# Kernel tuning notes

Hardware: AMD Instinct MI355X
Metric: run time of the kernel (lower is better)

## Reference

```python
import jax, jax.numpy as jnp
import numpy as np

N_NODES = 50000
N_EDGES = 800000
NODE_DIM = 256
EDGE_DIM = 64
NUM_REL = 4
HID = 512      # hidden_dims[0]
LAST = 128     # last_dim_size
BATCH = 16384
EPS = 1e-10    # torchdrug RelationalGraphConv degree-normalization eps


def _glorot(k, shape):
    fan_in = shape[-1]
    return jax.random.normal(k, shape, jnp.float32) / np.sqrt(fan_in).astype(np.float32)


def setup_inputs() -> dict:
    key = jax.random.key(0)
    ks = jax.random.split(key, 20)
    inp = {}
    inp["inputs"] = jax.random.randint(ks[0], (BATCH, 3), 0, N_NODES, dtype=jnp.int32)
    inp["node_feature"] = jax.random.normal(ks[1], (N_NODES, NODE_DIM), jnp.float32)
    inp["edge_feature"] = jax.random.normal(ks[2], (N_EDGES, EDGE_DIM), jnp.float32)
    inp["edge_src"] = jax.random.randint(ks[3], (N_EDGES,), 0, N_NODES, dtype=jnp.int32)
    inp["edge_dst"] = jax.random.randint(ks[4], (N_EDGES,), 0, N_NODES, dtype=jnp.int32)
    inp["edge_rel"] = jax.random.randint(ks[5], (N_EDGES,), 0, NUM_REL, dtype=jnp.int32)
    # RGCN layer 1: 256 -> 512
    inp["We1"] = _glorot(ks[6], (NODE_DIM, EDGE_DIM)); inp["be1"] = jnp.zeros((NODE_DIM,), jnp.float32)
    inp["Wl1"] = _glorot(ks[7], (HID, NUM_REL * NODE_DIM)); inp["bl1"] = jnp.zeros((HID,), jnp.float32)
    inp["Ws1"] = _glorot(ks[8], (HID, NODE_DIM)); inp["bs1"] = jnp.zeros((HID,), jnp.float32)
    # RGCN layer 2: 512 -> 128
    inp["We2"] = _glorot(ks[9], (HID, EDGE_DIM)); inp["be2"] = jnp.zeros((HID,), jnp.float32)
    inp["Wl2"] = _glorot(ks[10], (LAST, NUM_REL * HID)); inp["bl2"] = jnp.zeros((LAST,), jnp.float32)
    inp["Ws2"] = _glorot(ks[11], (LAST, HID)); inp["bs2"] = jnp.zeros((LAST,), jnp.float32)
    # ccle_mlp: edge_dim -> 256 -> 128
    inp["Wc1"] = _glorot(ks[12], (256, EDGE_DIM)); inp["bc1"] = jnp.zeros((256,), jnp.float32)
    inp["Wc2"] = _glorot(ks[13], (LAST, 256)); inp["bc2"] = jnp.zeros((LAST,), jnp.float32)
    # final MLP: 3*128 -> 128 -> 64 -> 1
    inp["Wf1"] = _glorot(ks[14], (128, 3 * LAST)); inp["bf1"] = jnp.zeros((128,), jnp.float32)
    inp["Wf2"] = _glorot(ks[15], (64, 128)); inp["bf2"] = jnp.zeros((64,), jnp.float32)
    inp["Wf3"] = _glorot(ks[16], (1, 64)); inp["bf3"] = jnp.zeros((1,), jnp.float32)
    return inp


def _rgcn_layer(x, edge_src, edge_dst, edge_rel, edge_feat, We, be, Wl, bl, Ws, bs):
    """torchdrug RelationalGraphConv: message = x[src] + edge_linear(edge_feat);
    per-(node,relation) mean aggregation; combine = linear(update) + self_loop(x); relu."""
    in_dim = x.shape[1]
    msg = x[edge_src] + edge_feat @ We.T + be                      # [E, in_dim]
    seg = edge_dst * NUM_REL + edge_rel                            # [E]
    agg = jax.ops.segment_sum(msg, seg, num_segments=N_NODES * NUM_REL)
    cnt = jax.ops.segment_sum(jnp.ones((msg.shape[0], 1), msg.dtype), seg,
                              num_segments=N_NODES * NUM_REL)
    upd = (agg / (cnt + EPS)).reshape(N_NODES, NUM_REL * in_dim)   # [N, R*in_dim]
    return jax.nn.relu(upd @ Wl.T + bl + x @ Ws.T + bs)


def reference(inputs, node_feature, edge_feature, edge_src, edge_dst, edge_rel,
              We1, be1, Wl1, bl1, Ws1, bs1,
              We2, be2, Wl2, bl2, Ws2, bs2,
              Wc1, bc1, Wc2, bc2,
              Wf1, bf1, Wf2, bf2, Wf3, bf3):
    d1, d2, ctx = inputs[:, 0], inputs[:, 1], inputs[:, 2]
    h = _rgcn_layer(node_feature, edge_src, edge_dst, edge_rel, edge_feature,
                    We1, be1, Wl1, bl1, Ws1, bs1)
    h = _rgcn_layer(h, edge_src, edge_dst, edge_rel, edge_feature,
                    We2, be2, Wl2, bl2, Ws2, bs2)
    x1 = h[d1]                                                     # [B, 128]
    x2 = h[d2]                                                     # [B, 128]
    ef = edge_feature[ctx]                                         # [B, 64]
    x3 = jax.nn.relu(ef @ Wc1.T + bc1) @ Wc2.T + bc2               # [B, 128]
    x = jnp.concatenate([x1, x2, x3], axis=1)                      # [B, 384]
    x = jax.nn.relu(x @ Wf1.T + bf1)
    x = jax.nn.relu(x @ Wf2.T + bf2)
    return x @ Wf3.T + bf3                                         # [B, 1]
```

## Files before the change

kernel.cpp:

```cpp
#include <hip/hip_runtime.h>
#include <hip/hip_bf16.h>

#define N_NODES 50000
#define N_EDGES 800000
#define NODE_DIM 256
#define EDGE_DIM 64
#define NUM_REL 4
#define HID 512
#define LAST 128
#define BATCH 16384
#define EPS 1e-10f
#define NSEG (N_NODES * NUM_REL)

#define K1 1600
#define K2 832

typedef __bf16 bf16_t;
typedef __attribute__((ext_vector_type(8))) __bf16 bf16x8;
typedef __attribute__((ext_vector_type(4))) __bf16 bf16x4;
typedef __attribute__((ext_vector_type(2))) __bf16 bf16x2;
typedef __attribute__((ext_vector_type(4))) float f32x4;

typedef __attribute__((address_space(1))) const unsigned int g_u32;
typedef __attribute__((address_space(3))) unsigned int l_u32;
static __device__ __forceinline__ void gload16(const void* g, void* l) {
    __builtin_amdgcn_global_load_lds((g_u32*)g, (l_u32*)l, 16, 0, 0);
}

__global__ __launch_bounds__(256) void hist_kernel(
    const int* __restrict__ edst, const int* __restrict__ erel, int* __restrict__ hist)
{
    int e = blockIdx.x * 256 + threadIdx.x;
    if (e >= N_EDGES) return;
    atomicAdd(&hist[edst[e] * NUM_REL + erel[e]], 1);
}

#define SCAN_B 2048
__global__ __launch_bounds__(256) void scan1(
    const int* __restrict__ in, int* __restrict__ out, int* __restrict__ bsum, int n)
{
    __shared__ int sh[256];
    int base = blockIdx.x * SCAN_B + threadIdx.x * 8;
    int v[8]; int s = 0;
#pragma unroll
    for (int i = 0; i < 8; ++i) {
        int idx = base + i;
        v[i] = s;
        s += (idx < n) ? in[idx] : 0;
    }
    sh[threadIdx.x] = s;
    __syncthreads();
    for (int off = 1; off < 256; off <<= 1) {
        int t = (threadIdx.x >= off) ? sh[threadIdx.x - off] : 0;
        __syncthreads();
        sh[threadIdx.x] += t;
        __syncthreads();
    }
    int texcl = (threadIdx.x == 0) ? 0 : sh[threadIdx.x - 1];
#pragma unroll
    for (int i = 0; i < 8; ++i) {
        int idx = base + i;
        if (idx < n) out[idx] = texcl + v[i];
    }
    if (threadIdx.x == 255) bsum[blockIdx.x] = sh[255];
}

__global__ void scan2(int* bsum, int nb)
{
    if (threadIdx.x == 0 && blockIdx.x == 0) {
        int s = 0;
        for (int i = 0; i < nb; ++i) { int t = bsum[i]; bsum[i] = s; s += t; }
    }
}

__global__ __launch_bounds__(256) void scan3(int* __restrict__ out, int* __restrict__ cursor,
                                             const int* __restrict__ bsum, int n)
{
    int idx = blockIdx.x * SCAN_B + threadIdx.x * 8;
    int add = bsum[blockIdx.x];
#pragma unroll
    for (int i = 0; i < 8; ++i)
        if (idx + i < n) {
            int v = out[idx + i] + add;
            out[idx + i] = v;
            cursor[idx + i] = v;
        }
}

__global__ __launch_bounds__(256) void csr_fill(
    const int* __restrict__ edst, const int* __restrict__ erel, const int* __restrict__ esrc,
    int* __restrict__ cursor,
    int* __restrict__ csr_src, int* __restrict__ csr_eid)
{
    int e = blockIdx.x * 256 + threadIdx.x;
    if (e >= N_EDGES) return;
    int seg = edst[e] * NUM_REL + erel[e];
    int pos = atomicAdd(&cursor[seg], 1);
    csr_src[pos] = esrc[e];
    csr_eid[pos] = e;
}

__global__ __launch_bounds__(256) void prep_small(
    const float* __restrict__ Wc1, const float* __restrict__ Wc2,
    const float* __restrict__ Wf1, const float* __restrict__ Wf2,
    const float* __restrict__ bl1, const float* __restrict__ bs1,
    const float* __restrict__ bl2, const float* __restrict__ bs2,
    bf16_t* __restrict__ Wc1b, bf16_t* __restrict__ Wc2b,
    bf16_t* __restrict__ Wf1b, bf16_t* __restrict__ Wf2b,
    float* __restrict__ bias12, float* __restrict__ bias22)
{
    int i = blockIdx.x * 256 + threadIdx.x;
    const float* src; bf16_t* dst; int base;
    if (i < 4096)        { src = Wc1; dst = Wc1b; base = 0; }
    else if (i < 12288)  { src = Wc2; dst = Wc2b; base = 4096; }
    else if (i < 24576)  { src = Wf1; dst = Wf1b; base = 12288; }
    else if (i < 26624)  { src = Wf2; dst = Wf2b; base = 24576; }
    else {
        int j = i - 26624;
        if (j < 512) bias12[j] = bl1[j] + bs1[j];
        else if (j < 640) bias22[j - 512] = bl2[j - 512] + bs2[j - 512];
        return;
    }
    int k = i - base;
    float4 v = ((const float4*)src)[k];
    bf16x4 o;
    o[0] = (bf16_t)v.x; o[1] = (bf16_t)v.y; o[2] = (bf16_t)v.z; o[3] = (bf16_t)v.w;
    ((bf16x4*)dst)[k] = o;
}

__global__ __launch_bounds__(256) void xconv_k(const float* __restrict__ x, bf16_t* __restrict__ A1,
                                               bf16_t* __restrict__ xb)
{
    int i = blockIdx.x * 256 + threadIdx.x;
    int n = i >> 6;
    int c4 = i & 63;
    float4 v = ((const float4*)(x + (size_t)n * 256))[c4];
    bf16x4 o;
    o[0] = (bf16_t)v.x; o[1] = (bf16_t)v.y; o[2] = (bf16_t)v.z; o[3] = (bf16_t)v.w;
    *(bf16x4*)(A1 + (size_t)n * K1 + 1280 + c4 * 4) = o;
    *(bf16x4*)(xb + (size_t)n * 256 + c4 * 4) = o;
}

__global__ __launch_bounds__(256) void prep_w1cat(
    const float* __restrict__ Wl1, const float* __restrict__ We1,
    const float* __restrict__ Ws1, const float* __restrict__ be1, bf16_t* __restrict__ W1cat)
{
    int j = blockIdx.x;
    int t = threadIdx.x;
    const float* wrow = Wl1 + (size_t)j * 1024;
    bf16_t* out = W1cat + (size_t)j * K1;
    for (int c = t; c < 1024; c += 256) out[c] = (bf16_t)wrow[c];
    {
        int r = t >> 6, e = t & 63;
        float s = 0.f;
        const float* wr = wrow + r * 256;
        for (int c = 0; c < 256; ++c) s += wr[c] * We1[c * 64 + e];
        out[1024 + t] = (bf16_t)s;
    }
    if (t < 256) out[1280 + t] = (bf16_t)Ws1[(size_t)j * 256 + t];
    if (t < 4) {
        float s = 0.f;
        const float* wr = wrow + t * 256;
        for (int c = 0; c < 256; ++c) s += wr[c] * be1[c];
        out[1536 + t] = (bf16_t)s;
    }
    if (t >= 4 && t < 64) out[1536 + t] = (bf16_t)0.f;
}

__global__ __launch_bounds__(256) void prep_w2cat(
    const float* __restrict__ Wl2, const float* __restrict__ We2,
    const float* __restrict__ Ws2, const float* __restrict__ be2, bf16_t* __restrict__ W2cat)
{
    int j = blockIdx.x;
    int t = threadIdx.x;
    const float* wrow = Wl2 + (size_t)j * 2048;
    bf16_t* out = W2cat + (size_t)j * K2;
    {
        int r = t >> 6, e = t & 63;
        float s = 0.f;
        const float* wr = wrow + r * 512;
        for (int k = 0; k < 512; ++k) s += wr[k] * We2[k * 64 + e];
        out[t] = (bf16_t)s;
    }
    for (int c = t; c < 512; c += 256) out[256 + c] = (bf16_t)Ws2[(size_t)j * 512 + c];
    if (t < 4) {
        float s = 0.f;
        const float* wr = wrow + t * 512;
        for (int k = 0; k < 512; ++k) s += wr[k] * be2[k];
        out[768 + t] = (bf16_t)s;
    }
    if (t >= 4 && t < 64) out[768 + t] = (bf16_t)0.f;
}

__global__ __launch_bounds__(256) void prep_w2p(const float* __restrict__ Wl2, bf16_t* __restrict__ W2p)
{
    int idx = blockIdx.x * 256 + threadIdx.x;
    int row = idx >> 9, k = idx & 511;
    int j = row & 127, r = row >> 7;
    W2p[idx] = (bf16_t)Wl2[(size_t)j * 2048 + r * 512 + k];
}

__global__ __launch_bounds__(256) void agg1(
    const float* __restrict__ ef, const bf16_t* __restrict__ xb,
    const int* __restrict__ csr_src, const int* __restrict__ csr_eid,
    const int* __restrict__ offs, const int* __restrict__ hist,
    bf16_t* __restrict__ A1, bf16_t* __restrict__ A2)
{
    int n = blockIdx.x;
    int w = threadIdx.x >> 6;
    int lane = threadIdx.x & 63;
    int half = lane >> 5;
    int l32 = lane & 31;
    int seg = n * NUM_REL + w;
    int beg = offs[seg], ct = hist[seg];

    float xs[8] = {0.f, 0.f, 0.f, 0.f, 0.f, 0.f, 0.f, 0.f};
    float es0 = 0.f, es1 = 0.f;

    int i = 0;
    for (; i + 4 <= ct; i += 4) {
        int sA = csr_src[beg + i + half];
        int sB = csr_src[beg + i + 2 + half];
        int eA = csr_eid[beg + i + half];
        int eB = csr_eid[beg + i + 2 + half];
        bf16x8 vA = *(const bf16x8*)(xb + (size_t)sA * 256 + l32 * 8);
        bf16x8 vB = *(const bf16x8*)(xb + (size_t)sB * 256 + l32 * 8);
        float2 fA = *(const float2*)(ef + (size_t)eA * 64 + l32 * 2);
        float2 fB = *(const float2*)(ef + (size_t)eB * 64 + l32 * 2);
#pragma unroll
        for (int j = 0; j < 8; ++j) xs[j] += (float)vA[j] + (float)vB[j];
        es0 += fA.x + fB.x;
        es1 += fA.y + fB.y;
    }
    for (; i + 2 <= ct; i += 2) {
        int sA = csr_src[beg + i + half];
        int eA = csr_eid[beg + i + half];
        bf16x8 vA = *(const bf16x8*)(xb + (size_t)sA * 256 + l32 * 8);
        float2 fA = *(const float2*)(ef + (size_t)eA * 64 + l32 * 2);
#pragma unroll
        for (int j = 0; j < 8; ++j) xs[j] += (float)vA[j];
        es0 += fA.x;
        es1 += fA.y;
    }
    if (i < ct && half == 0) {
        int sA = csr_src[beg + i];
        int eA = csr_eid[beg + i];
        bf16x8 vA = *(const bf16x8*)(xb + (size_t)sA * 256 + l32 * 8);
        float2 fA = *(const float2*)(ef + (size_t)eA * 64 + l32 * 2);
#pragma unroll
        for (int j = 0; j < 8; ++j) xs[j] += (float)vA[j];
        es0 += fA.x;
        es1 += fA.y;
    }
#pragma unroll
    for (int j = 0; j < 8; ++j) xs[j] += __shfl_xor(xs[j], 32);
    es0 += __shfl_xor(es0, 32);
    es1 += __shfl_xor(es1, 32);

    float inv = 1.0f / ((float)ct + EPS);
    if (half == 0) {
        bf16x8 m;
#pragma unroll
        for (int j = 0; j < 8; ++j) m[j] = (bf16_t)(xs[j] * inv);
        *(bf16x8*)(A1 + (size_t)n * K1 + w * 256 + l32 * 8) = m;
        bf16x2 e2;
        e2[0] = (bf16_t)(es0 * inv);
        e2[1] = (bf16_t)(es1 * inv);
        *(bf16x2*)(A1 + (size_t)n * K1 + 1024 + w * 64 + l32 * 2) = e2;
        *(bf16x2*)(A2 + (size_t)n * K2 + w * 64 + l32 * 2) = e2;
    }
    if (lane == 0) {
        bf16_t fv = (bf16_t)((float)ct * inv);
        A1[(size_t)n * K1 + 1536 + w] = fv;
        A2[(size_t)n * K2 + 768 + w] = fv;
    }
    if (w == 3 && lane >= 4) {
        A1[(size_t)n * K1 + 1536 + lane] = (bf16_t)0.f;
        A2[(size_t)n * K2 + 768 + lane] = (bf16_t)0.f;
    }
}

__global__ __launch_bounds__(256) void agg2(
    const bf16_t* __restrict__ P, const int* __restrict__ csr_src,
    const int* __restrict__ offs, const int* __restrict__ hist,
    float* __restrict__ h2base)
{
    __shared__ float red[4][128];
    int n = blockIdx.x;
    int w = threadIdx.x >> 6;
    int lane = threadIdx.x & 63;
    int half = lane >> 5;
    int l32 = lane & 31;
    int seg = n * NUM_REL + w;
    int beg = offs[seg], ct = hist[seg];

    float s0 = 0.f, s1 = 0.f, s2 = 0.f, s3 = 0.f;
    int i = 0;
    for (; i + 4 <= ct; i += 4) {
        int a = csr_src[beg + i + half];
        int b = csr_src[beg + i + 2 + half];
        bf16x4 va = *(const bf16x4*)(P + (size_t)a * HID + w * 128 + l32 * 4);
        bf16x4 vb = *(const bf16x4*)(P + (size_t)b * HID + w * 128 + l32 * 4);
        s0 += (float)va[0] + (float)vb[0];
        s1 += (float)va[1] + (float)vb[1];
        s2 += (float)va[2] + (float)vb[2];
        s3 += (float)va[3] + (float)vb[3];
    }
    for (; i + 2 <= ct; i += 2) {
        int a = csr_src[beg + i + half];
        bf16x4 va = *(const bf16x4*)(P + (size_t)a * HID + w * 128 + l32 * 4);
        s0 += (float)va[0]; s1 += (float)va[1]; s2 += (float)va[2]; s3 += (float)va[3];
    }
    if (i < ct && half == 0) {
        int a = csr_src[beg + i];
        bf16x4 va = *(const bf16x4*)(P + (size_t)a * HID + w * 128 + l32 * 4);
        s0 += (float)va[0]; s1 += (float)va[1]; s2 += (float)va[2]; s3 += (float)va[3];
    }
    s0 += __shfl_xor(s0, 32);
    s1 += __shfl_xor(s1, 32);
    s2 += __shfl_xor(s2, 32);
    s3 += __shfl_xor(s3, 32);

    float inv = 1.0f / ((float)ct + EPS);
    if (half == 0) {
        red[w][l32 * 4 + 0] = s0 * inv;
        red[w][l32 * 4 + 1] = s1 * inv;
        red[w][l32 * 4 + 2] = s2 * inv;
        red[w][l32 * 4 + 3] = s3 * inv;
    }
    __syncthreads();
    int t = threadIdx.x;
    if (t < 128)
        h2base[(size_t)n * 128 + t] = red[0][t] + red[1][t] + red[2][t] + red[3][t];
}

template<int RELU, int ACC, int OUTBF>
__global__ __launch_bounds__(256) void gemm_bf16(
    const bf16_t* __restrict__ A, int lda,
    const bf16_t* __restrict__ W, int ldw,
    const float* __restrict__ Cin, int ldcin,
    const float* __restrict__ bias,
    void* __restrict__ Cout, int ldc,
    int M, int N, int K, int ncol)
{
    __shared__ char smem[65536];
    const int tid = threadIdx.x;

    const int nwg = gridDim.x;
    const int q8 = nwg >> 3, r8 = nwg & 7;
    const int xcd = blockIdx.x & 7, li = blockIdx.x >> 3;
    const int wgid = (xcd < r8 ? xcd * (q8 + 1) : r8 * (q8 + 1) + (xcd - r8) * q8) + li;

    const int row0 = (wgid / ncol) * 128;
    const int col0 = (wgid % ncol) * 128;
    const int lane = tid & 63, wv = tid >> 6;

    const int rsub = lane >> 3;
    const int gchunk = (lane & 7) ^ rsub;
    const bf16_t* pa[4]; const bf16_t* pb[4];
    int lofs[4];
#pragma unroll
    for (int s = 0; s < 4; ++s) {
        int q = wv * 4 + s;
        int ar = row0 + q * 8 + rsub; if (ar >= M) ar = M - 1;
        int br = col0 + q * 8 + rsub; if (br >= N) br = N - 1;
        pa[s] = A + (size_t)ar * lda + gchunk * 8;
        pb[s] = W + (size_t)br * ldw + gchunk * 8;
        lofs[s] = q * 1024;
    }

    const int wm = wv >> 1, wn = wv & 1;
    const int r16 = lane & 15, kch = lane >> 4;
    const int sw = r16 & 7;

    f32x4 acc[4][4];
#pragma unroll
    for (int i = 0; i < 4; ++i)
#pragma unroll
        for (int j = 0; j < 4; ++j) acc[i][j] = (f32x4){0.f, 0.f, 0.f, 0.f};

#pragma unroll
    for (int s = 0; s < 4; ++s) {
        gload16(pa[s], smem + lofs[s]);
        gload16(pb[s], smem + 16384 + lofs[s]);
    }

    const int nk = K >> 6;
    int cur = 0;
    for (int it = 0; it < nk; ++it) {
        const int k0 = it << 6;
        if (it + 1 < nk) {
            char* nb = smem + ((cur ^ 1) << 15);
#pragma unroll
            for (int s = 0; s < 4; ++s) {
                gload16(pa[s] + k0 + 64, nb + lofs[s]);
                gload16(pb[s] + k0 + 64, nb + 16384 + lofs[s]);
            }
            asm volatile("s_waitcnt vmcnt(8)" ::: "memory");
        } else {
            asm volatile("s_waitcnt vmcnt(0)" ::: "memory");
        }
        __builtin_amdgcn_s_barrier();
        __builtin_amdgcn_sched_barrier(0);
        const char* As = smem + (cur << 15);
        const char* Bs = As + 16384;
#pragma unroll
        for (int t = 0; t < 2; ++t) {
            const int slot = ((t * 4 + kch) ^ sw) << 4;
            bf16x8 af[4], bfm[4];
#pragma unroll
            for (int i = 0; i < 4; ++i)
                af[i] = *(const bf16x8*)(As + (wm * 64 + i * 16 + r16) * 128 + slot);
#pragma unroll
            for (int j = 0; j < 4; ++j)
                bfm[j] = *(const bf16x8*)(Bs + (wn * 64 + j * 16 + r16) * 128 + slot);
#pragma unroll
            for (int i = 0; i < 4; ++i)
#pragma unroll
                for (int j = 0; j < 4; ++j)
                    acc[i][j] = __builtin_amdgcn_mfma_f32_16x16x32_bf16(af[i], bfm[j], acc[i][j], 0, 0, 0);
        }
        __builtin_amdgcn_s_barrier();
        cur ^= 1;
    }

    const int crow0 = row0 + wm * 64;
#pragma unroll
    for (int i = 0; i < 4; ++i) {
#pragma unroll
        for (int j = 0; j < 4; ++j) {
            int col = col0 + wn * 64 + j * 16 + r16;
            if (col >= N) continue;
            float bv = bias ? bias[col] : 0.f;
#pragma unroll
            for (int q = 0; q < 4; ++q) {
                int row = crow0 + i * 16 + kch * 4 + q;
                if (row >= M) continue;
                float v = acc[i][j][q] + bv;
                if (ACC) v += Cin[(size_t)row * ldcin + col];
                if (RELU) v = fmaxf(v, 0.f);
                if (OUTBF) ((bf16_t*)Cout)[(size_t)row * ldc + col] = (bf16_t)v;
                else       ((float*)Cout)[(size_t)row * ldc + col] = v;
            }
        }
    }
}

__global__ __launch_bounds__(256) void gemm_f1g(
    const int* __restrict__ inputs, const bf16_t* __restrict__ h2,
    const bf16_t* __restrict__ x3, const bf16_t* __restrict__ Wf1b,
    const float* __restrict__ bf1, bf16_t* __restrict__ f1)
{
    __shared__ char smem[65536];
    const int tid = threadIdx.x;
    const int nwg = gridDim.x;
    const int q8 = nwg >> 3;
    const int xcd = blockIdx.x & 7, li = blockIdx.x >> 3;
    const int wgid = xcd * q8 + li;
    const int row0 = wgid * 128;
    const int lane = tid & 63, wv = tid >> 6;

    const int rsub = lane >> 3;
    const int gchunk = (lane & 7) ^ rsub;
    const bf16_t* baseA[4][3];
    const bf16_t* pb[4];
    int lofs[4];
#pragma unroll
    for (int s = 0; s < 4; ++s) {
        int q = wv * 4 + s;
        int ar = row0 + q * 8 + rsub;
        int d1 = inputs[ar * 3 + 0];
        int d2 = inputs[ar * 3 + 1];
        baseA[s][0] = h2 + (size_t)d1 * 128 + gchunk * 8;
        baseA[s][1] = h2 + (size_t)d2 * 128 + gchunk * 8;
        baseA[s][2] = x3 + (size_t)ar * 128 + gchunk * 8;
        int br = q * 8 + rsub;
        pb[s] = Wf1b + (size_t)br * 384 + gchunk * 8;
        lofs[s] = q * 1024;
    }

    const int wm = wv >> 1, wn = wv & 1;
    const int r16 = lane & 15, kch = lane >> 4;
    const int sw = r16 & 7;

    f32x4 acc[4][4];
#pragma unroll
    for (int i = 0; i < 4; ++i)
#pragma unroll
        for (int j = 0; j < 4; ++j) acc[i][j] = (f32x4){0.f, 0.f, 0.f, 0.f};

#pragma unroll
    for (int s = 0; s < 4; ++s) {
        gload16(baseA[s][0], smem + lofs[s]);
        gload16(pb[s], smem + 16384 + lofs[s]);
    }

    int cur = 0;
#pragma unroll
    for (int it = 0; it < 6; ++it) {
        const int k0 = it << 6;
        if (it < 5) {
            const int kn = k0 + 64;
            const int reg = kn >> 7, off = kn & 127;
            char* nb = smem + ((cur ^ 1) << 15);
#pragma unroll
            for (int s = 0; s < 4; ++s) {
                gload16(baseA[s][reg] + off, nb + lofs[s]);
                gload16(pb[s] + kn, nb + 16384 + lofs[s]);
            }
            asm volatile("s_waitcnt vmcnt(8)" ::: "memory");
        } else {
            asm volatile("s_waitcnt vmcnt(0)" ::: "memory");
        }
        __builtin_amdgcn_s_barrier();
        __builtin_amdgcn_sched_barrier(0);
        const char* As = smem + (cur << 15);
        const char* Bs = As + 16384;
#pragma unroll
        for (int t = 0; t < 2; ++t) {
            const int slot = ((t * 4 + kch) ^ sw) << 4;
            bf16x8 af[4], bfm[4];
#pragma unroll
            for (int i = 0; i < 4; ++i)
                af[i] = *(const bf16x8*)(As + (wm * 64 + i * 16 + r16) * 128 + slot);
#pragma unroll
            for (int j = 0; j < 4; ++j)
                bfm[j] = *(const bf16x8*)(Bs + (wn * 64 + j * 16 + r16) * 128 + slot);
#pragma unroll
            for (int i = 0; i < 4; ++i)
#pragma unroll
                for (int j = 0; j < 4; ++j)
                    acc[i][j] = __builtin_amdgcn_mfma_f32_16x16x32_bf16(af[i], bfm[j], acc[i][j], 0, 0, 0);
        }
        __builtin_amdgcn_s_barrier();
        cur ^= 1;
    }

    const int crow0 = row0 + wm * 64;
#pragma unroll
    for (int i = 0; i < 4; ++i) {
#pragma unroll
        for (int j = 0; j < 4; ++j) {
            int col = wn * 64 + j * 16 + r16;
            if (col >= 128) continue;
            float bv = bf1[col];
#pragma unroll
            for (int q = 0; q < 4; ++q) {
                int row = crow0 + i * 16 + kch * 4 + q;
                float v = fmaxf(acc[i][j][q] + bv, 0.f);
                f1[(size_t)row * 128 + col] = (bf16_t)v;
            }
        }
    }
}

__global__ __launch_bounds__(256) void gather_ef(
    const int* __restrict__ inputs, const float* __restrict__ ef, bf16_t* __restrict__ ef_g)
{
    int i = blockIdx.x * 256 + threadIdx.x;
    int row = i >> 4, c4 = i & 15;
    int ctx = inputs[row * 3 + 2];
    float4 v = *(const float4*)(ef + (size_t)ctx * 64 + c4 * 4);
    bf16x4 o;
    o[0] = (bf16_t)v.x; o[1] = (bf16_t)v.y; o[2] = (bf16_t)v.z; o[3] = (bf16_t)v.w;
    *(bf16x4*)(ef_g + (size_t)row * 64 + c4 * 4) = o;
}

__global__ __launch_bounds__(256) void head_tail(
    const bf16_t* __restrict__ f1, const bf16_t* __restrict__ Wf2b,
    const float* __restrict__ bf2, const float* __restrict__ Wf3,
    const float* __restrict__ bf3, float* __restrict__ out)
{
    __shared__ bf16_t sf1[128 * 128];
    int blk = blockIdx.x;
    int tid = threadIdx.x;
    const bf16_t* gsrc = f1 + (size_t)blk * 128 * 128;
    for (int i = tid; i < 128 * 16; i += 256)
        ((bf16x8*)sf1)[i] = ((const bf16x8*)gsrc)[i];
    int lane = tid & 63, wv = tid >> 6;
    bf16x8 w[16];
#pragma unroll
    for (int c = 0; c < 16; ++c) w[c] = ((const bf16x8*)(Wf2b + lane * 128))[c];
    float bias2 = bf2[lane];
    float wf3 = Wf3[lane];
    float b3 = bf3[0];
    __syncthreads();
    for (int r = wv; r < 128; r += 4) {
        const bf16x8* frow = (const bf16x8*)(sf1 + r * 128);
        float acc = 0.f;
#pragma unroll
        for (int c = 0; c < 16; ++c) {
            bf16x8 fv = frow[c];
#pragma unroll
            for (int j = 0; j < 8; ++j) acc += (float)fv[j] * (float)w[c][j];
        }
        float v = fmaxf(acc + bias2, 0.f) * wf3;
#pragma unroll
        for (int off = 32; off > 0; off >>= 1) v += __shfl_down(v, off);
        if (lane == 0) out[blk * 128 + r] = v + b3;
    }
}

extern "C" void kernel_launch(void* const* d_in, const int* in_sizes, int n_in,
                              void* d_out, int out_size, void* d_ws, size_t ws_size,
                              hipStream_t stream)
{
    const int*   inputs       = (const int*)  d_in[0];
    const float* node_feature = (const float*)d_in[1];
    const float* edge_feature = (const float*)d_in[2];
    const int*   edge_src     = (const int*)  d_in[3];
    const int*   edge_dst     = (const int*)  d_in[4];
    const int*   edge_rel     = (const int*)  d_in[5];
    const float* We1 = (const float*)d_in[6];
    const float* be1 = (const float*)d_in[7];
    const float* Wl1 = (const float*)d_in[8];
    const float* bl1 = (const float*)d_in[9];
    const float* Ws1 = (const float*)d_in[10];
    const float* bs1 = (const float*)d_in[11];
    const float* We2 = (const float*)d_in[12];
    const float* be2 = (const float*)d_in[13];
    const float* Wl2 = (const float*)d_in[14];
    const float* bl2 = (const float*)d_in[15];
    const float* Ws2 = (const float*)d_in[16];
    const float* bs2 = (const float*)d_in[17];
    const float* Wc1 = (const float*)d_in[18];
    const float* bc1 = (const float*)d_in[19];
    const float* Wc2 = (const float*)d_in[20];
    const float* bc2 = (const float*)d_in[21];
    const float* Wf1 = (const float*)d_in[22];
    const float* bf1 = (const float*)d_in[23];
    const float* Wf2 = (const float*)d_in[24];
    const float* bf2 = (const float*)d_in[25];
    const float* Wf3 = (const float*)d_in[26];
    const float* bf3 = (const float*)d_in[27];
    float* out = (float*)d_out;

    char* p = (char*)d_ws;
    auto alloc = [&](size_t bytes) { char* r = p; p += (bytes + 255) & ~(size_t)255; return r; };
    int* hist     = (int*)alloc(NSEG * 4);
    int* offs     = (int*)alloc(NSEG * 4);
    int* cursor   = (int*)alloc(NSEG * 4);
    int* csr_src  = (int*)alloc(N_EDGES * 4);
    int* csr_eid  = (int*)alloc(N_EDGES * 4);
    int* bsums    = (int*)alloc(128 * 4);
    bf16_t* A1    = (bf16_t*)alloc((size_t)N_NODES * K1 * 2);
    bf16_t* A2    = (bf16_t*)alloc((size_t)N_NODES * K2 * 2);
    bf16_t* xb    = (bf16_t*)alloc((size_t)N_NODES * 256 * 2);
    bf16_t* Pbuf  = (bf16_t*)alloc((size_t)N_NODES * HID * 2);
    float*  h2base= (float*)alloc((size_t)N_NODES * 128 * 4);
    bf16_t* h2    = (bf16_t*)alloc((size_t)N_NODES * 128 * 2);
    bf16_t* W1cat = (bf16_t*)alloc((size_t)512 * K1 * 2);
    bf16_t* W2cat = (bf16_t*)alloc((size_t)128 * K2 * 2);
    bf16_t* W2p   = (bf16_t*)alloc((size_t)512 * 512 * 2);
    bf16_t* Wc1b  = (bf16_t*)alloc(256 * 64 * 2);
    bf16_t* Wc2b  = (bf16_t*)alloc(128 * 256 * 2);
    bf16_t* Wf1b  = (bf16_t*)alloc(128 * 384 * 2);
    bf16_t* Wf2b  = (bf16_t*)alloc(64 * 128 * 2);
    float*  bias12= (float*)alloc(512 * 4);
    float*  bias22= (float*)alloc(128 * 4);
    bf16_t* ef_g  = (bf16_t*)alloc((size_t)BATCH * 64 * 2);
    bf16_t* u3    = (bf16_t*)alloc((size_t)BATCH * 256 * 2);
    bf16_t* x3buf = (bf16_t*)alloc((size_t)BATCH * 128 * 2);
    bf16_t* f1    = (bf16_t*)alloc((size_t)BATCH * 128 * 2);

    hipMemsetAsync(hist, 0, NSEG * 4, stream);
    hist_kernel<<<(N_EDGES + 255) / 256, 256, 0, stream>>>(edge_dst, edge_rel, hist);
    int nscan = (NSEG + SCAN_B - 1) / SCAN_B;
    scan1<<<nscan, 256, 0, stream>>>(hist, offs, bsums, NSEG);
    scan2<<<1, 64, 0, stream>>>(bsums, nscan);
    scan3<<<nscan, 256, 0, stream>>>(offs, cursor, bsums, NSEG);
    csr_fill<<<(N_EDGES + 255) / 256, 256, 0, stream>>>(edge_dst, edge_rel, edge_src,
                                                        cursor, csr_src, csr_eid);

    prep_w1cat<<<512, 256, 0, stream>>>(Wl1, We1, Ws1, be1, W1cat);
    prep_w2cat<<<128, 256, 0, stream>>>(Wl2, We2, Ws2, be2, W2cat);
    prep_w2p<<<(512 * 512) / 256, 256, 0, stream>>>(Wl2, W2p);
    prep_small<<<(26624 + 640 + 255) / 256, 256, 0, stream>>>(
        Wc1, Wc2, Wf1, Wf2, bl1, bs1, bl2, bs2,
        Wc1b, Wc2b, Wf1b, Wf2b, bias12, bias22);
    xconv_k<<<(N_NODES * 64 + 255) / 256, 256, 0, stream>>>(node_feature, A1, xb);

    agg1<<<N_NODES, 256, 0, stream>>>(edge_feature, xb, csr_src, csr_eid, offs, hist, A1, A2);
    {
        int nrow = (N_NODES + 127) / 128, ncol = HID / 128;
        gemm_bf16<1, 0, 1><<<nrow * ncol, 256, 0, stream>>>(A1, K1, W1cat, K1, nullptr, 0, bias12,
                                                            A2 + 256, K2, N_NODES, HID, K1, ncol);
    }

    {
        int nrow = (N_NODES + 127) / 128, ncol = HID / 128;
        gemm_bf16<0, 0, 1><<<nrow * ncol, 256, 0, stream>>>(A2 + 256, K2, W2p, 512, nullptr, 0, nullptr,
                                                            Pbuf, HID, N_NODES, HID, 512, ncol);
    }
    agg2<<<N_NODES, 256, 0, stream>>>(Pbuf, csr_src, offs, hist, h2base);
    {
        int nrow = (N_NODES + 127) / 128;
        gemm_bf16<1, 1, 1><<<nrow, 256, 0, stream>>>(A2, K2, W2cat, K2, h2base, 128, bias22,
                                                     h2, 128, N_NODES, 128, K2, 1);
    }

    gather_ef<<<(BATCH * 16) / 256, 256, 0, stream>>>(inputs, edge_feature, ef_g);
    {
        gemm_bf16<1, 0, 1><<<(BATCH / 128) * 2, 256, 0, stream>>>(ef_g, 64, Wc1b, 64, nullptr, 0, bc1,
                                                                  u3, 256, BATCH, 256, 64, 2);
    }
    {
        gemm_bf16<0, 0, 1><<<BATCH / 128, 256, 0, stream>>>(u3, 256, Wc2b, 256, nullptr, 0, bc2,
                                                            x3buf, 128, BATCH, 128, 256, 1);
    }
    gemm_f1g<<<BATCH / 128, 256, 0, stream>>>(inputs, h2, x3buf, Wf1b, bf1, f1);
    head_tail<<<BATCH / 128, 256, 0, stream>>>(f1, Wf2b, bf2, Wf3, bf3, out);
}
```

Baseline: 694.0 us.

## Replace double-buffered 64-K GEMM pipeline with single-buffered 32-K tiles

Both bf16 GEMM kernels drop the double-buffered LDS pipeline with 64-wide K steps and use a single 16KB buffer with 32-wide K steps, synchronised by __syncthreads around each step. The LDS swizzle is reworked for 64-byte rows. This cuts LDS use per workgroup from 64KB to 16KB, which may let more workgroups share a CU. In exchange, global loads no longer overlap with MFMA work and each K step needs two barriers, so latency is exposed more often.

```diff
diff --git a/kernel.cpp b/kernel.cpp
--- a/kernel.cpp
+++ b/kernel.cpp
@@ -343,7 +343,7 @@
     void* __restrict__ Cout, int ldc,
     int M, int N, int K, int ncol)
 {
-    __shared__ char smem[65536];
+    __shared__ char smem[16384];
     const int tid = threadIdx.x;
 
     const int nwg = gridDim.x;
@@ -355,23 +355,31 @@
     const int col0 = (wgid % ncol) * 128;
     const int lane = tid & 63, wv = tid >> 6;
 
-    const int rsub = lane >> 3;
-    const int gchunk = (lane & 7) ^ rsub;
-    const bf16_t* pa[4]; const bf16_t* pb[4];
-    int lofs[4];
-#pragma unroll
-    for (int s = 0; s < 4; ++s) {
-        int q = wv * 4 + s;
-        int ar = row0 + q * 8 + rsub; if (ar >= M) ar = M - 1;
-        int br = col0 + q * 8 + rsub; if (br >= N) br = N - 1;
-        pa[s] = A + (size_t)ar * lda + gchunk * 8;
-        pb[s] = W + (size_t)br * ldw + gchunk * 8;
-        lofs[s] = q * 1024;
-    }
+    const int srow = lane >> 2;
+    const int gchunk = (lane & 3) ^ ((lane >> 3) & 3);
+    const bf16_t *pa0, *pa1, *pb0, *pb1;
+    {
+        int r0 = (wv * 2 + 0) * 16 + srow;
+        int r1 = (wv * 2 + 1) * 16 + srow;
+        int a0 = row0 + r0; if (a0 >= M) a0 = M - 1;
+        int a1 = row0 + r1; if (a1 >= M) a1 = M - 1;
+        int b0 = col0 + r0; if (b0 >= N) b0 = N - 1;
+        int b1 = col0 + r1; if (b1 >= N) b1 = N - 1;
+        pa0 = A + (size_t)a0 * lda + gchunk * 8;
+        pa1 = A + (size_t)a1 * lda + gchunk * 8;
+        pb0 = W + (size_t)b0 * ldw + gchunk * 8;
+        pb1 = W + (size_t)b1 * ldw + gchunk * 8;
+    }
+    char* As = smem;
+    char* Bs = smem + 8192;
+    char* lA0 = As + (wv * 2 + 0) * 1024;
+    char* lA1 = As + (wv * 2 + 1) * 1024;
+    char* lB0 = Bs + (wv * 2 + 0) * 1024;
+    char* lB1 = Bs + (wv * 2 + 1) * 1024;
 
     const int wm = wv >> 1, wn = wv & 1;
     const int r16 = lane & 15, kch = lane >> 4;
-    const int sw = r16 & 7;
+    const int slot = (kch ^ ((r16 >> 1) & 3)) << 4;
 
     f32x4 acc[4][4];
 #pragma unroll
@@ -379,49 +387,25 @@
 #pragma unroll
         for (int j = 0; j < 4; ++j) acc[i][j] = (f32x4){0.f, 0.f, 0.f, 0.f};
 
-#pragma unroll
-    for (int s = 0; s < 4; ++s) {
-        gload16(pa[s], smem + lofs[s]);
-        gload16(pb[s], smem + 16384 + lofs[s]);
-    }
-
-    const int nk = K >> 6;
-    int cur = 0;
-    for (int it = 0; it < nk; ++it) {
-        const int k0 = it << 6;
-        if (it + 1 < nk) {
-            char* nb = smem + ((cur ^ 1) << 15);
-#pragma unroll
-            for (int s = 0; s < 4; ++s) {
-                gload16(pa[s] + k0 + 64, nb + lofs[s]);
-                gload16(pb[s] + k0 + 64, nb + 16384 + lofs[s]);
-            }
-            asm volatile("s_waitcnt vmcnt(8)" ::: "memory");
-        } else {
-            asm volatile("s_waitcnt vmcnt(0)" ::: "memory");
-        }
-        __builtin_amdgcn_s_barrier();
-        __builtin_amdgcn_sched_barrier(0);
-        const char* As = smem + (cur << 15);
-        const char* Bs = As + 16384;
-#pragma unroll
-        for (int t = 0; t < 2; ++t) {
-            const int slot = ((t * 4 + kch) ^ sw) << 4;
-            bf16x8 af[4], bfm[4];
-#pragma unroll
-            for (int i = 0; i < 4; ++i)
-                af[i] = *(const bf16x8*)(As + (wm * 64 + i * 16 + r16) * 128 + slot);
+    for (int k0 = 0; k0 < K; k0 += 32) {
+        gload16(pa0 + k0, lA0);
+        gload16(pa1 + k0, lA1);
+        gload16(pb0 + k0, lB0);
+        gload16(pb1 + k0, lB1);
+        __syncthreads();
+        bf16x8 af[4], bfm[4];
+#pragma unroll
+        for (int i = 0; i < 4; ++i)
+            af[i] = *(const bf16x8*)(As + (wm * 64 + i * 16 + r16) * 64 + slot);
+#pragma unroll
+        for (int j = 0; j < 4; ++j)
+            bfm[j] = *(const bf16x8*)(Bs + (wn * 64 + j * 16 + r16) * 64 + slot);
+#pragma unroll
+        for (int i = 0; i < 4; ++i)
 #pragma unroll
             for (int j = 0; j < 4; ++j)
-                bfm[j] = *(const bf16x8*)(Bs + (wn * 64 + j * 16 + r16) * 128 + slot);
-#pragma unroll
-            for (int i = 0; i < 4; ++i)
-#pragma unroll
-                for (int j = 0; j < 4; ++j)
-                    acc[i][j] = __builtin_amdgcn_mfma_f32_16x16x32_bf16(af[i], bfm[j], acc[i][j], 0, 0, 0);
-        }
-        __builtin_amdgcn_s_barrier();
-        cur ^= 1;
+                acc[i][j] = __builtin_amdgcn_mfma_f32_16x16x32_bf16(af[i], bfm[j], acc[i][j], 0, 0, 0);
+        __syncthreads();
     }
 
     const int crow0 = row0 + wm * 64;
@@ -451,37 +435,46 @@
     const bf16_t* __restrict__ x3, const bf16_t* __restrict__ Wf1b,
     const float* __restrict__ bf1, bf16_t* __restrict__ f1)
 {
-    __shared__ char smem[65536];
+    __shared__ char smem[16384];
     const int tid = threadIdx.x;
     const int nwg = gridDim.x;
-    const int q8 = nwg >> 3;
+    const int q8n = nwg >> 3;
     const int xcd = blockIdx.x & 7, li = blockIdx.x >> 3;
-    const int wgid = xcd * q8 + li;
+    const int wgid = xcd * q8n + li;
     const int row0 = wgid * 128;
     const int lane = tid & 63, wv = tid >> 6;
 
-    const int rsub = lane >> 3;
-    const int gchunk = (lane & 7) ^ rsub;
-    const bf16_t* baseA[4][3];
-    const bf16_t* pb[4];
-    int lofs[4];
-#pragma unroll
-    for (int s = 0; s < 4; ++s) {
-        int q = wv * 4 + s;
-        int ar = row0 + q * 8 + rsub;
-        int d1 = inputs[ar * 3 + 0];
-        int d2 = inputs[ar * 3 + 1];
-        baseA[s][0] = h2 + (size_t)d1 * 128 + gchunk * 8;
-        baseA[s][1] = h2 + (size_t)d2 * 128 + gchunk * 8;
-        baseA[s][2] = x3 + (size_t)ar * 128 + gchunk * 8;
-        int br = q * 8 + rsub;
-        pb[s] = Wf1b + (size_t)br * 384 + gchunk * 8;
-        lofs[s] = q * 1024;
-    }
+    const int srow = lane >> 2;
+    const int gchunk = (lane & 3) ^ ((lane >> 3) & 3);
+    const bf16_t* baseA0[3];
+    const bf16_t* baseA1[3];
+    const bf16_t *pb0, *pb1;
+    {
+        int r0 = (wv * 2 + 0) * 16 + srow;
+        int r1 = (wv * 2 + 1) * 16 + srow;
+        int ar0 = row0 + r0;
+        int ar1 = row0 + r1;
+        int d10 = inputs[ar0 * 3 + 0], d20 = inputs[ar0 * 3 + 1];
+        int d11 = inputs[ar1 * 3 + 0], d21 = inputs[ar1 * 3 + 1];
+        baseA0[0] = h2 + (size_t)d10 * 128 + gchunk * 8;
+        baseA0[1] = h2 + (size_t)d20 * 128 + gchunk * 8;
+        baseA0[2] = x3 + (size_t)ar0 * 128 + gchunk * 8;
+        baseA1[0] = h2 + (size_t)d11 * 128 + gchunk * 8;
+        baseA1[1] = h2 + (size_t)d21 * 128 + gchunk * 8;
+        baseA1[2] = x3 + (size_t)ar1 * 128 + gchunk * 8;
+        pb0 = Wf1b + (size_t)r0 * 384 + gchunk * 8;
+        pb1 = Wf1b + (size_t)r1 * 384 + gchunk * 8;
+    }
+    char* As = smem;
+    char* Bs = smem + 8192;
+    char* lA0 = As + (wv * 2 + 0) * 1024;
+    char* lA1 = As + (wv * 2 + 1) * 1024;
+    char* lB0 = Bs + (wv * 2 + 0) * 1024;
+    char* lB1 = Bs + (wv * 2 + 1) * 1024;
 
     const int wm = wv >> 1, wn = wv & 1;
     const int r16 = lane & 15, kch = lane >> 4;
-    const int sw = r16 & 7;
+    const int slot = (kch ^ ((r16 >> 1) & 3)) << 4;
 
     f32x4 acc[4][4];
 #pragma unroll
@@ -490,50 +483,28 @@
         for (int j = 0; j < 4; ++j) acc[i][j] = (f32x4){0.f, 0.f, 0.f, 0.f};
 
 #pragma unroll
-    for (int s = 0; s < 4; ++s) {
-        gload16(baseA[s][0], smem + lofs[s]);
-        gload16(pb[s], smem + 16384 + lofs[s]);
-    }
-
-    int cur = 0;
-#pragma unroll
-    for (int it = 0; it < 6; ++it) {
-        const int k0 = it << 6;
-        if (it < 5) {
-            const int kn = k0 + 64;
-            const int reg = kn >> 7, off = kn & 127;
-            char* nb = smem + ((cur ^ 1) << 15);
-#pragma unroll
-            for (int s = 0; s < 4; ++s) {
-                gload16(baseA[s][reg] + off, nb + lofs[s]);
-                gload16(pb[s] + kn, nb + 16384 + lofs[s]);
-            }
-            asm volatile("s_waitcnt vmcnt(8)" ::: "memory");
-        } else {
-            asm volatile("s_waitcnt vmcnt(0)" ::: "memory");
-        }
-        __builtin_amdgcn_s_barrier();
-        __builtin_amdgcn_sched_barrier(0);
-        const char* As = smem + (cur << 15);
-        const char* Bs = As + 16384;
-#pragma unroll
-        for (int t = 0; t < 2; ++t) {
-            const int slot = ((t * 4 + kch) ^ sw) << 4;
-            bf16x8 af[4], bfm[4];
-#pragma unroll
-            for (int i = 0; i < 4; ++i)
-                af[i] = *(const bf16x8*)(As + (wm * 64 + i * 16 + r16) * 128 + slot);
+    for (int it = 0; it < 12; ++it) {
+        const int k0 = it * 32;
+        const int reg = k0 >> 7;
+        const int off = k0 & 127;
+        gload16(baseA0[reg] + off, lA0);
+        gload16(baseA1[reg] + off, lA1);
+        gload16(pb0 + k0, lB0);
+        gload16(pb1 + k0, lB1);
+        __syncthreads();
+        bf16x8 af[4], bfm[4];
+#pragma unroll
+        for (int i = 0; i < 4; ++i)
+            af[i] = *(const bf16x8*)(As + (wm * 64 + i * 16 + r16) * 64 + slot);
+#pragma unroll
+        for (int j = 0; j < 4; ++j)
+            bfm[j] = *(const bf16x8*)(Bs + (wn * 64 + j * 16 + r16) * 64 + slot);
+#pragma unroll
+        for (int i = 0; i < 4; ++i)
 #pragma unroll
             for (int j = 0; j < 4; ++j)
-                bfm[j] = *(const bf16x8*)(Bs + (wn * 64 + j * 16 + r16) * 128 + slot);
-#pragma unroll
-            for (int i = 0; i < 4; ++i)
-#pragma unroll
-                for (int j = 0; j < 4; ++j)
-                    acc[i][j] = __builtin_amdgcn_mfma_f32_16x16x32_bf16(af[i], bfm[j], acc[i][j], 0, 0, 0);
-        }
-        __builtin_amdgcn_s_barrier();
-        cur ^= 1;
+                acc[i][j] = __builtin_amdgcn_mfma_f32_16x16x32_bf16(af[i], bfm[j], acc[i][j], 0, 0, 0);
+        __syncthreads();
     }
 
     const int crow0 = row0 + wm * 64;
@@ -542,7 +513,6 @@
 #pragma unroll
         for (int j = 0; j < 4; ++j) {
             int col = wn * 64 + j * 16 + r16;
-            if (col >= 128) continue;
             float bv = bf1[col];
 #pragma unroll
             for (int q = 0; q < 4; ++q) {
```

Result: slower. 748.0 us (+7.8%).

## Add 256x256-tile triple-buffered GEMM kernel for the two large node GEMMs

Applied to the files above, without the earlier changes.

Introduces a new 512-thread GEMM kernel with 256x256 output tiles, a three-stage LDS ring buffer with BK=32, split A/B global loads interleaved with MFMA phases, and s_setprio around the MFMA blocks. It replaces the 128x128 kernel for the layer-1 GEMM (K=1600) and the layer-2 projection GEMM. The larger tile raises arithmetic intensity and cuts redundant global reads of A and W. In exchange it uses 96KB of LDS and 128 accumulator registers per thread, which limits occupancy, and only about 196x2 workgroups are launched for 256 CUs, so the wave quantization may be poor. It also drops a column guard in the f1 epilogue.

```diff
diff --git a/kernel.cpp b/kernel.cpp
--- a/kernel.cpp
+++ b/kernel.cpp
@@ -334,6 +334,135 @@
         h2base[(size_t)n * 128 + t] = red[0][t] + red[1][t] + red[2][t] + red[3][t];
 }
 
+template<int RELU>
+__global__ __launch_bounds__(512) void gemm256(
+    const bf16_t* __restrict__ A, int lda,
+    const bf16_t* __restrict__ W, int ldw,
+    const float* __restrict__ bias,
+    bf16_t* __restrict__ Cout, int ldc,
+    int M, int N, int K, int ncol)
+{
+    __shared__ char smem[98304];
+    const int tid = threadIdx.x;
+
+    const int nwg = gridDim.x;
+    const int q8 = nwg >> 3, r8 = nwg & 7;
+    const int xcd = blockIdx.x & 7, li = blockIdx.x >> 3;
+    const int wgid = (xcd < r8 ? xcd * (q8 + 1) : r8 * (q8 + 1) + (xcd - r8) * q8) + li;
+
+    const int row0 = (wgid / ncol) * 256;
+    const int col0 = (wgid % ncol) * 256;
+    const int lane = tid & 63, wv = tid >> 6;
+
+    const int rsub = lane >> 2;
+    const int gc = (lane & 3) ^ ((lane >> 3) & 3);
+    const bf16_t *pa[2], *pb[2];
+    int lof[2];
+#pragma unroll
+    for (int s = 0; s < 2; ++s) {
+        int g = wv * 2 + s;
+        int ar = row0 + g * 16 + rsub; if (ar >= M) ar = M - 1;
+        int br = col0 + g * 16 + rsub; if (br >= N) br = N - 1;
+        pa[s] = A + (size_t)ar * lda + gc * 8;
+        pb[s] = W + (size_t)br * ldw + gc * 8;
+        lof[s] = g * 1024;
+    }
+
+    const int wm = wv >> 2, wn = wv & 3;
+    const int r16 = lane & 15, kch = lane >> 4;
+    const int slot = (kch ^ ((r16 >> 1) & 3)) << 4;
+
+    f32x4 acc[8][4];
+#pragma unroll
+    for (int i = 0; i < 8; ++i)
+#pragma unroll
+        for (int j = 0; j < 4; ++j) acc[i][j] = (f32x4){0.f, 0.f, 0.f, 0.f};
+
+    const int nt = K >> 5;
+#pragma unroll
+    for (int t = 0; t < 2; ++t) {
+        char* b = smem + t * 32768;
+        gload16(pa[0] + t * 32, b + lof[0]);
+        gload16(pa[1] + t * 32, b + lof[1]);
+        gload16(pb[0] + t * 32, b + 16384 + lof[0]);
+        gload16(pb[1] + t * 32, b + 16384 + lof[1]);
+    }
+    asm volatile("s_waitcnt vmcnt(4)" ::: "memory");
+    __builtin_amdgcn_s_barrier();
+
+    for (int t = 0; t < nt; ++t) {
+        char* buf = smem + (t % 3) * 32768;
+        char* nbuf = smem + ((t + 2) % 3) * 32768;
+        const bool st = (t + 2 < nt);
+        const int k2 = (t + 2) * 32;
+
+        bf16x8 bA[4], bB[4];
+#pragma unroll
+        for (int i = 0; i < 4; ++i)
+            bA[i] = *(const bf16x8*)(buf + (wm * 128 + i * 16 + r16) * 64 + slot);
+#pragma unroll
+        for (int j = 0; j < 4; ++j)
+            bB[j] = *(const bf16x8*)(buf + 16384 + (wn * 64 + j * 16 + r16) * 64 + slot);
+        if (st) {
+            gload16(pa[0] + k2, nbuf + lof[0]);
+            gload16(pa[1] + k2, nbuf + lof[1]);
+        }
+        __builtin_amdgcn_s_barrier();
+        asm volatile("s_waitcnt lgkmcnt(0)" ::: "memory");
+        __builtin_amdgcn_sched_barrier(0);
+        __builtin_amdgcn_s_setprio(1);
+#pragma unroll
+        for (int i = 0; i < 4; ++i)
+#pragma unroll
+            for (int j = 0; j < 4; ++j)
+                acc[i][j] = __builtin_amdgcn_mfma_f32_16x16x32_bf16(bA[i], bB[j], acc[i][j], 0, 0, 0);
+        __builtin_amdgcn_s_setprio(0);
+        __builtin_amdgcn_s_barrier();
+
+        bf16x8 aH[4];
+#pragma unroll
+        for (int i = 0; i < 4; ++i)
+            aH[i] = *(const bf16x8*)(buf + (wm * 128 + 64 + i * 16 + r16) * 64 + slot);
+        if (st) {
+            gload16(pb[0] + k2, nbuf + 16384 + lof[0]);
+            gload16(pb[1] + k2, nbuf + 16384 + lof[1]);
+        }
+        __builtin_amdgcn_s_barrier();
+        asm volatile("s_waitcnt lgkmcnt(0)" ::: "memory");
+        __builtin_amdgcn_sched_barrier(0);
+        __builtin_amdgcn_s_setprio(1);
+#pragma unroll
+        for (int i = 0; i < 4; ++i)
+#pragma unroll
+            for (int j = 0; j < 4; ++j)
+                acc[4 + i][j] = __builtin_amdgcn_mfma_f32_16x16x32_bf16(aH[i], bB[j], acc[4 + i][j], 0, 0, 0);
+        __builtin_amdgcn_s_setprio(0);
+        if (t + 1 < nt) {
+            if (st) asm volatile("s_waitcnt vmcnt(4)" ::: "memory");
+            else    asm volatile("s_waitcnt vmcnt(0)" ::: "memory");
+        }
+        __builtin_amdgcn_s_barrier();
+    }
+
+    const int crow0 = row0 + wm * 128;
+#pragma unroll
+    for (int i = 0; i < 8; ++i) {
+#pragma unroll
+        for (int j = 0; j < 4; ++j) {
+            int col = col0 + wn * 64 + j * 16 + r16;
+            float bv = bias ? bias[col] : 0.f;
+#pragma unroll
+            for (int q = 0; q < 4; ++q) {
+                int row = crow0 + i * 16 + kch * 4 + q;
+                if (row >= M) continue;
+                float v = acc[i][j][q] + bv;
+                if (RELU) v = fmaxf(v, 0.f);
+                Cout[(size_t)row * ldc + col] = (bf16_t)v;
+            }
+        }
+    }
+}
+
 template<int RELU, int ACC, int OUTBF>
 __global__ __launch_bounds__(256) void gemm_bf16(
     const bf16_t* __restrict__ A, int lda,
@@ -542,7 +671,6 @@
 #pragma unroll
         for (int j = 0; j < 4; ++j) {
             int col = wn * 64 + j * 16 + r16;
-            if (col >= 128) continue;
             float bv = bf1[col];
 #pragma unroll
             for (int q = 0; q < 4; ++q) {
@@ -682,15 +810,15 @@
 
     agg1<<<N_NODES, 256, 0, stream>>>(edge_feature, xb, csr_src, csr_eid, offs, hist, A1, A2);
     {
-        int nrow = (N_NODES + 127) / 128, ncol = HID / 128;
-        gemm_bf16<1, 0, 1><<<nrow * ncol, 256, 0, stream>>>(A1, K1, W1cat, K1, nullptr, 0, bias12,
-                                                            A2 + 256, K2, N_NODES, HID, K1, ncol);
+        int nrow = (N_NODES + 255) / 256, ncol = HID / 256;
+        gemm256<1><<<nrow * ncol, 512, 0, stream>>>(A1, K1, W1cat, K1, bias12,
+                                                    A2 + 256, K2, N_NODES, HID, K1, ncol);
     }
 
     {
-        int nrow = (N_NODES + 127) / 128, ncol = HID / 128;
-        gemm_bf16<0, 0, 1><<<nrow * ncol, 256, 0, stream>>>(A2 + 256, K2, W2p, 512, nullptr, 0, nullptr,
-                                                            Pbuf, HID, N_NODES, HID, 512, ncol);
+        int nrow = (N_NODES + 255) / 256, ncol = HID / 256;
+        gemm256<0><<<nrow * ncol, 512, 0, stream>>>(A2 + 256, K2, W2p, 512, nullptr,
+                                                    Pbuf, HID, N_NODES, HID, 512, ncol);
     }
     agg2<<<N_NODES, 256, 0, stream>>>(Pbuf, csr_src, offs, hist, h2base);
     {
```

New measurement: 692.2 us, median of 2. Within noise of the previous version (-0.3%).
